# Optimization experiments

Hardware: AMD Instinct MI355X
Metric: run time of the kernel (lower is better)

The kernel has to match this reference:

```python
import jax, jax.numpy as jnp
import numpy as np

K = 50          # NEC paper uses p=50 neighbors
DELTA = 1e-3    # kernel smoothing constant


def setup_inputs() -> dict:
    key = jax.random.key(0)
    ks = jax.random.split(key, 8)
    B, D_IN, D, A, C = 512, 2, 128, 3, 200000
    s = lambda fan_in: 1.0 / np.sqrt(fan_in)
    return {
        "x": jax.random.normal(ks[0], (B, D_IN), jnp.float32),
        "W1": jax.random.normal(ks[1], (D_IN, D), jnp.float32) * s(D_IN),
        "b1": jnp.zeros((D,), jnp.float32),
        "W2": jax.random.normal(ks[2], (D, D), jnp.float32) * s(D),
        "b2": jnp.zeros((D,), jnp.float32),
        "W3": jax.random.normal(ks[3], (D, D), jnp.float32) * s(D),
        "b3": jnp.zeros((D,), jnp.float32),
        "W4": jax.random.normal(ks[4], (D, D), jnp.float32) * s(D),
        "b4": jnp.zeros((D,), jnp.float32),
        "keys": jax.random.normal(ks[5], (A, C, D), jnp.float32),
        "mem_values": jax.random.normal(ks[6], (A, C), jnp.float32),
    }


def _encode(x, W1, b1, W2, b2, W3, b3, W4, b4):
    h = jax.nn.relu(x @ W1 + b1)
    h = jax.nn.relu(h @ W2 + b2)
    h = jax.nn.relu(h @ W3 + b3)
    return h @ W4 + b4  # [B, D]


def _dnd_lookup(h, keys, mem_values):
    # h: [B, D]; keys: [A, C, D]; mem_values: [A, C]
    q2 = jnp.sum(h * h, axis=-1)                       # [B]
    k2 = jnp.sum(keys * keys, axis=-1)                 # [A, C]
    cross = jnp.einsum("bd,acd->bac", h, keys)         # [B, A, C]
    d2 = jnp.maximum(q2[:, None, None] + k2[None] - 2.0 * cross, 0.0)
    neg_d, idx = jax.lax.top_k(-d2, K)                  # [B, A, K]
    d_top = -neg_d
    w = 1.0 / (d_top + DELTA)                           # NEC kernel
    w = w / jnp.sum(w, axis=-1, keepdims=True)
    a_idx = jnp.arange(keys.shape[0])[None, :, None]    # [1, A, 1]
    v_top = mem_values[a_idx, idx]                      # gather -> [B, A, K]
    values = jnp.sum(w * v_top, axis=-1)                # [B, A]
    return values


def reference(x, W1, b1, W2, b2, W3, b3, W4, b4, keys, mem_values):
    h = _encode(x, W1, b1, W2, b2, W3, b3, W4, b4)
    values = _dnd_lookup(h, keys, mem_values)
    actions = jnp.argmax(values, axis=-1)
    return values, actions
```

## Files before the change

### kernel.cpp

```cpp
#include <hip/hip_runtime.h>
#include <hip/hip_bf16.h>
#include <math.h>

#define B_    512
#define DIM   128
#define A_    3
#define C_    200000
#define K_    50
#define DELTA 1e-3

typedef __attribute__((ext_vector_type(8))) short bf16x8;
typedef __attribute__((ext_vector_type(4))) float f32x4;

#define NBIN_A 128
#define CAP_A  1024
#define NSEG_G 128
#define TPS_G  13
#define NT_G   1563
#define HSEG   16
#define CHPS   782
#define ROWCH  12500
#define NL     16

#define AOFF_H64   0u
#define AOFF_H32   524288u
#define AOFF_HBF   786432u
#define AOFF_Q2    917504u
#define AOFF_HIST  919552u
#define AOFF_CNT   1705984u
#define AOFF_TAUB  1712128u
#define AOFF_V64   1718272u
#define AOFF_CAND  1730560u
#define AOFF_BINS  8022016u
#define NEED_A     (8022016ull + 307200000ull)

#define NBIN_B 192
#define CAP_B  768
#define BM_B   64
#define BN_B   128
#define TPC_B  16
#define CHUNK_B (TPC_B*BN_B)
#define NCH_B  ((C_ + CHUNK_B - 1)/CHUNK_B)

#define BOFF_H32   0u
#define BOFF_H64   262144u
#define BOFF_Q2    786432u
#define BOFF_K2    788480u
#define BOFF_HIST  3188480u
#define BOFF_TAU   4368128u
#define BOFF_CNT   4374272u
#define BOFF_V64   4380416u
#define BOFF_CAND  4392704u

static __device__ inline unsigned short f2bf(float x) {
    union { float f; unsigned u; } c; c.f = x;
    unsigned r = (c.u + 0x7FFFu + ((c.u >> 16) & 1u)) >> 16;
    return (unsigned short)r;
}
static __device__ inline unsigned pkbf(float a, float b) {
    __hip_bfloat162 t = __float22bfloat162_rn(make_float2(a, b));
    union { __hip_bfloat162 h; unsigned u; } cv; cv.h = t; return cv.u;
}

__global__ __launch_bounds__(128) void mlp_kernel(
    const float* __restrict__ x,
    const float* __restrict__ W1, const float* __restrict__ b1,
    const float* __restrict__ W2, const float* __restrict__ b2,
    const float* __restrict__ W3, const float* __restrict__ b3,
    const float* __restrict__ W4, const float* __restrict__ b4,
    float* __restrict__ h32, unsigned short* __restrict__ hbf,
    double* __restrict__ h64, float* __restrict__ q2)
{
    int b = blockIdx.x, t = threadIdx.x;
    __shared__ double s0[DIM], s1[DIM];
    double x0 = (double)x[b*2+0], x1 = (double)x[b*2+1];
    double h = x0*(double)W1[t] + x1*(double)W1[DIM+t] + (double)b1[t];
    s0[t] = h > 0.0 ? h : 0.0;
    __syncthreads();
    double acc = (double)b2[t];
    for (int k = 0; k < DIM; k++) acc += s0[k]*(double)W2[k*DIM+t];
    s1[t] = acc > 0.0 ? acc : 0.0;
    __syncthreads();
    acc = (double)b3[t];
    for (int k = 0; k < DIM; k++) acc += s1[k]*(double)W3[k*DIM+t];
    s0[t] = acc > 0.0 ? acc : 0.0;
    __syncthreads();
    acc = (double)b4[t];
    for (int k = 0; k < DIM; k++) acc += s0[k]*(double)W4[k*DIM+t];
    h64[b*DIM+t] = acc;
    float hf = (float)acc;
    h32[b*DIM+t] = hf;
    hbf[b*DIM+t] = f2bf(hf);
    s1[t] = acc*acc;
    __syncthreads();
    for (int s = 64; s > 0; s >>= 1) { if (t < s) s1[t] += s1[t+s]; __syncthreads(); }
    if (t == 0) q2[b] = (float)s1[0];
}

__global__ __launch_bounds__(256, 2) void gemm_bin_kernel(
    const float* __restrict__ keys, const unsigned short* __restrict__ hbf,
    const float* __restrict__ q2, unsigned char* __restrict__ bins)
{
    const int seg = blockIdx.x, my = blockIdx.y, a = blockIdx.z;
    const int b0 = my*128;
    const int tid = threadIdx.x;
    const int lane = tid & 63, w = tid >> 6;
    const int lm = lane & 15, kh = lane >> 4;
    const int wm = w & 1;
    const int wn = w >> 1;

    __shared__ short sA[128*136];
    __shared__ short sB[128*136];
    __shared__ __align__(16) float q2s[128];
    __shared__ __align__(16) float k2s[128];

    {
        int r = tid >> 1, hh = tid & 1;
        const int4* gp = (const int4*)hbf + (size_t)(b0 + r)*16 + hh*8;
        int4* dp = (int4*)&sB[r*136 + hh*64];
        #pragma unroll
        for (int q = 0; q < 8; q++) dp[q] = gp[q];
        if (tid < 128) q2s[tid] = q2[b0 + tid];
    }

    for (int t = 0; t < TPS_G; t++) {
        int nt = seg*TPS_G + t;
        if (nt >= NT_G) break;
        int n0 = nt*128;
        __syncthreads();
        {
            int r = tid >> 1, hh = tid & 1;
            int nr = n0 + r; if (nr >= C_) nr = C_-1;
            const float4* gp = (const float4*)(keys + ((size_t)a*C_ + nr)*128) + hh*16;
            float ss = 0.0f;
            int4* dp = (int4*)&sA[r*136 + hh*64];
            #pragma unroll
            for (int q = 0; q < 8; q++) {
                float4 v0 = gp[2*q], v1 = gp[2*q+1];
                ss += v0.x*v0.x + v0.y*v0.y + v0.z*v0.z + v0.w*v0.w
                    + v1.x*v1.x + v1.y*v1.y + v1.z*v1.z + v1.w*v1.w;
                int4 pk;
                pk.x = (int)pkbf(v0.x, v0.y);
                pk.y = (int)pkbf(v0.z, v0.w);
                pk.z = (int)pkbf(v1.x, v1.y);
                pk.w = (int)pkbf(v1.z, v1.w);
                dp[q] = pk;
            }
            ss += __shfl_xor(ss, 1, 64);
            if (hh == 0) k2s[r] = ss;
        }
        __syncthreads();

        f32x4 acc[4][4];
        #pragma unroll
        for (int i = 0; i < 4; i++)
            #pragma unroll
            for (int j = 0; j < 4; j++) acc[i][j] = (f32x4){0.f, 0.f, 0.f, 0.f};

        #pragma unroll
        for (int kst = 0; kst < 4; kst++) {
            bf16x8 af[4], bfv[4];
            #pragma unroll
            for (int i = 0; i < 4; i++)
                af[i] = *(const bf16x8*)&sA[(wm*64 + i*16 + lm)*136 + kst*32 + kh*8];
            #pragma unroll
            for (int j = 0; j < 4; j++)
                bfv[j] = *(const bf16x8*)&sB[(wn*64 + j*16 + lm)*136 + kst*32 + kh*8];
            #pragma unroll
            for (int i = 0; i < 4; i++)
                #pragma unroll
                for (int j = 0; j < 4; j++)
                    acc[i][j] = __builtin_amdgcn_mfma_f32_16x16x32_bf16(af[i], bfv[j], acc[i][j], 0, 0, 0);
        }

        float qv[4];
        #pragma unroll
        for (int j = 0; j < 4; j++) qv[j] = q2s[wn*64 + j*16 + lm];
        #pragma unroll
        for (int i = 0; i < 4; i++) {
            int nb = wm*64 + i*16 + kh*4;
            int n  = n0 + nb;
            float4 kb = *(const float4*)&k2s[nb];
            if (n < C_) {
                #pragma unroll
                for (int j = 0; j < 4; j++) {
                    int bl = wn*64 + j*16 + lm;
                    unsigned pk = 0;
                    #pragma unroll
                    for (int r = 0; r < 4; r++) {
                        float kr = (r==0 ? kb.x : r==1 ? kb.y : r==2 ? kb.z : kb.w);
                        float d2v = fmaf(-2.0f, acc[i][j][r], qv[j] + kr);
                        float dc  = fminf(fmaxf(d2v, 16.0f), 4095.0f);
                        unsigned u = (__float_as_uint(dc) >> 19) - 2096u;
                        pk |= u << (8*r);
                    }
                    *(unsigned*)(bins + ((size_t)(a*B_ + b0 + bl))*C_ + n) = pk;
                }
            }
        }
    }
}

__global__ __launch_bounds__(256) void histA_kernel(const unsigned char* __restrict__ bins,
                                                    unsigned* __restrict__ hist)
{
    int q = blockIdx.x;
    int seg = blockIdx.y;
    int tid = threadIdx.x;
    int a = q >> 9, b = q & 511;
    int p = b*A_ + a;
    __shared__ unsigned hs[NBIN_A*8];
    for (int i = tid; i < NBIN_A*8; i += 256) hs[i] = 0;
    __syncthreads();
    const uint4* row = (const uint4*)(bins + (size_t)q*C_);
    int ch0 = seg*CHPS, ch1 = ch0 + CHPS; if (ch1 > ROWCH) ch1 = ROWCH;
    int rep = tid & 7;
    for (int ch = ch0 + tid; ch < ch1; ch += 256) {
        uint4 v = row[ch];
        unsigned d[4] = {v.x, v.y, v.z, v.w};
        #pragma unroll
        for (int e = 0; e < 4; e++) {
            unsigned x = d[e];
            atomicAdd(&hs[((x      ) & 127u)*8 + rep], 1u);
            atomicAdd(&hs[((x >>  8) & 127u)*8 + rep], 1u);
            atomicAdd(&hs[((x >> 16) & 127u)*8 + rep], 1u);
            atomicAdd(&hs[((x >> 24) & 127u)*8 + rep], 1u);
        }
    }
    __syncthreads();
    if (tid < NBIN_A) {
        unsigned s = 0;
        #pragma unroll
        for (int r2 = 0; r2 < 8; r2++) s += hs[tid*8 + r2];
        if (s) atomicAdd(&hist[(size_t)p*NBIN_A + tid], s);
    }
}

__global__ void tauA_kernel(const unsigned* __restrict__ hist, int* __restrict__ taubin)
{
    int p = blockIdx.x*256 + threadIdx.x;
    if (p >= B_*A_) return;
    const unsigned* hp = hist + (size_t)p*NBIN_A;
    unsigned cum = 0; int jsel = NBIN_A-1;
    for (int j = 0; j < NBIN_A; j++) { cum += hp[j]; if (cum >= K_) { jsel = j; break; } }
    unsigned c1 = cum + (jsel+1 < NBIN_A ? hp[jsel+1] : 0u);
    unsigned c2 = c1  + (jsel+2 < NBIN_A ? hp[jsel+2] : 0u);
    int jt = (c2 <= 768u) ? jsel+2 : jsel+1;
    if (jt > NBIN_A-1) jt = NBIN_A-1;
    taubin[p] = jt;
}

__global__ __launch_bounds__(256) void collectA_kernel(const unsigned char* __restrict__ bins,
    const int* __restrict__ taubin, unsigned* __restrict__ cnt, int* __restrict__ cand)
{
    int q = blockIdx.x, seg = blockIdx.y, tid = threadIdx.x;
    int a = q >> 9, b = q & 511;
    int p = b*A_ + a;
    int tb = taubin[p];
    unsigned thr  = (unsigned)(tb + 1);
    unsigned addv = (128u - thr) * 0x01010101u;
    const uint4* row = (const uint4*)(bins + (size_t)q*C_);
    int ch0 = seg*CHPS, ch1 = ch0 + CHPS; if (ch1 > ROWCH) ch1 = ROWCH;
    for (int ch = ch0 + tid; ch < ch1; ch += 256) {
        uint4 v = row[ch];
        unsigned d[4] = {v.x, v.y, v.z, v.w};
        #pragma unroll
        for (int e = 0; e < 4; e++) {
            unsigned m = (d[e] + addv) & 0x80808080u;
            if (m != 0x80808080u) {
                #pragma unroll
                for (int by = 0; by < 4; by++) {
                    if (!((m >> (8*by + 7)) & 1u)) {
                        int n = ch*16 + e*4 + by;
                        unsigned pos = atomicAdd(&cnt[p], 1u);
                        if (pos < CAP_A) cand[(size_t)p*CAP_A + pos] = n;
                    }
                }
            }
        }
    }
}

__global__ __launch_bounds__(64) void select_kernel(
    const float* __restrict__ keys, const double* __restrict__ h64,
    const float* __restrict__ mem_values,
    const unsigned* __restrict__ cnt, const int* __restrict__ cand,
    float* __restrict__ out_values, double* __restrict__ val64, int cap)
{
    int p = blockIdx.x; int b = p / A_, a = p % A_;
    int lane = threadIdx.x;
    __shared__ double hd[DIM];
    __shared__ float  vsm[CAP_A];

    for (int i = lane; i < DIM; i += 64) hd[i] = h64[(size_t)b*DIM + i];
    int n = (int)cnt[p]; if (n > cap) n = cap;
    __syncthreads();

    double d2r[NL];
    #pragma unroll
    for (int s = 0; s < NL; s++) d2r[s] = 1e300;

    #pragma unroll 1
    for (int s = 0; s < NL; s++) {
        int i = s*64 + lane;
        if (i < n) {
            int c = cand[(size_t)p*cap + i];
            const float4* kr = (const float4*)(keys + ((size_t)a*C_ + c)*DIM);
            double s0 = 0.0, s1 = 0.0;
            #pragma unroll 4
            for (int kq = 0; kq < 32; kq++) {
                float4 kv = kr[kq];
                double d0 = hd[4*kq+0] - (double)kv.x;
                double d1 = hd[4*kq+1] - (double)kv.y;
                double d2 = hd[4*kq+2] - (double)kv.z;
                double d3 = hd[4*kq+3] - (double)kv.w;
                s0 += d0*d0 + d1*d1; s1 += d2*d2 + d3*d3;
            }
            double d = s0 + s1;
            unsigned long long bits = __double_as_longlong(d);
            bits = (bits & ~1023ull) | (unsigned long long)i;
            d2r[s] = __longlong_as_double(bits);
            vsm[i] = mem_values[(size_t)a*C_ + c];
        }
    }
    __syncthreads();

    double accw = 0.0, accwv = 0.0;
    for (int t = 0; t < K_; t++) {
        double best = d2r[0];
        #pragma unroll
        for (int s = 1; s < NL; s++) best = fmin(best, d2r[s]);
        #pragma unroll
        for (int off = 32; off > 0; off >>= 1) {
            double o = __shfl_xor(best, off, 64);
            best = fmin(best, o);
        }
        if (best >= 1e300) break;
        unsigned gidx = (unsigned)(__double_as_longlong(best) & 1023ull);
        int ol = gidx & 63, os = gidx >> 6;
        if (lane == ol) {
            #pragma unroll
            for (int s = 0; s < NL; s++) if (s == os) d2r[s] = 1e300;
        }
        double d = best; if (d < 0.0) d = 0.0;
        double wgt = 1.0 / (d + DELTA);
        accw += wgt; accwv += wgt * (double)vsm[gidx];
    }
    if (lane == 0) {
        double v = accwv / accw;
        out_values[p] = (float)v;
        val64[p] = v;
    }
}

__global__ void argmax_kernel(const double* __restrict__ val64, float* __restrict__ out)
{
    int b = blockIdx.x*blockDim.x + threadIdx.x;
    if (b >= B_) return;
    double v0 = val64[b*A_+0], v1 = val64[b*A_+1], v2 = val64[b*A_+2];
    int bi = 0; double bv = v0;
    if (v1 > bv) { bv = v1; bi = 1; }
    if (v2 > bv) { bv = v2; bi = 2; }
    out[B_*A_ + b] = (float)bi;
}

__global__ __launch_bounds__(256) void k2_kernel(const float* __restrict__ keys,
                                                 float* __restrict__ k2)
{
    int r = blockIdx.x*4 + (threadIdx.x >> 6);
    int lane = threadIdx.x & 63;
    float2 v = ((const float2*)keys)[(size_t)r*64 + lane];
    float s = v.x*v.x + v.y*v.y;
    #pragma unroll
    for (int off = 32; off > 0; off >>= 1) s += __shfl_down(s, off, 64);
    if (lane == 0) k2[r] = s;
}

template<int MODE>
__global__ __launch_bounds__(256) void pass_kernel(
    const float* __restrict__ keys, const float* __restrict__ h32,
    const float* __restrict__ q2,   const float* __restrict__ k2,
    unsigned* __restrict__ hist,    const float* __restrict__ tau,
    unsigned* __restrict__ cnt,     int* __restrict__ cand)
{
    const int bt = blockIdx.x;
    const int ch = blockIdx.y;
    const int a  = blockIdx.z;
    const int b0 = bt*BM_B;
    const int tid = threadIdx.x;
    const int tx = tid & 31, ty = tid >> 5;

    __shared__ float4 hs4[BM_B*33];
    __shared__ float4 ks4[BN_B*33];
    __shared__ float  q2s[BM_B];
    __shared__ float  taus[BM_B];
    __shared__ unsigned hist_s[MODE == 0 ? BM_B*NBIN_B : 1];

    #pragma unroll
    for (int q = 0; q < BM_B*32/256; q++) {
        int flat = q*256 + tid; int row = flat >> 5, kq = flat & 31;
        hs4[row*33 + kq] = ((const float4*)h32)[(size_t)(b0+row)*32 + kq];
    }
    if (tid < BM_B) {
        q2s[tid] = q2[b0+tid];
        if (MODE == 1) taus[tid] = tau[(b0+tid)*A_ + a];
    }
    if (MODE == 0) for (int i = tid; i < BM_B*NBIN_B; i += 256) hist_s[i] = 0;
    const float* __restrict__ k2g = k2 + (size_t)a*C_;

    for (int t = 0; t < TPC_B; t++) {
        int n0 = ch*CHUNK_B + t*BN_B;
        if (n0 >= C_) break;
        __syncthreads();
        #pragma unroll
        for (int q = 0; q < 16; q++) {
            int flat = q*256 + tid; int row = flat >> 5, kq = flat & 31;
            int nr = n0 + row; if (nr >= C_) nr = C_-1;
            ks4[row*33 + kq] = ((const float4*)keys)[((size_t)a*C_ + nr)*32 + kq];
        }
        __syncthreads();

        float acc[8][4];
        #pragma unroll
        for (int i = 0; i < 8; i++)
            #pragma unroll
            for (int j = 0; j < 4; j++) acc[i][j] = 0.0f;

        for (int kq = 0; kq < 32; kq++) {
            float4 hv[8], kv[4];
            #pragma unroll
            for (int i = 0; i < 8; i++) hv[i] = hs4[(ty*8+i)*33 + kq];
            #pragma unroll
            for (int j = 0; j < 4; j++) kv[j] = ks4[(j*32+tx)*33 + kq];
            #pragma unroll
            for (int i = 0; i < 8; i++)
                #pragma unroll
                for (int j = 0; j < 4; j++)
                    acc[i][j] += hv[i].x*kv[j].x + hv[i].y*kv[j].y
                               + hv[i].z*kv[j].z + hv[i].w*kv[j].w;
        }

        #pragma unroll
        for (int i = 0; i < 8; i++) {
            int bl = ty*8 + i;
            float q2b = q2s[bl];
            #pragma unroll
            for (int j = 0; j < 4; j++) {
                int n = n0 + j*32 + tx;
                if (n < C_) {
                    float d2f = fmaxf(q2b + k2g[n] - 2.0f*acc[i][j], 0.0f);
                    if (MODE == 0) {
                        int bin = (int)(__float_as_uint(d2f + 1.0f) >> 19) - 2032;
                        bin = bin < 0 ? 0 : (bin > NBIN_B-1 ? NBIN_B-1 : bin);
                        atomicAdd(&hist_s[bl*NBIN_B + bin], 1u);
                    } else {
                        if (d2f < taus[bl]) {
                            int p = (b0+bl)*A_ + a;
                            unsigned pos = atomicAdd(&cnt[p], 1u);
                            if (pos < CAP_B) cand[(size_t)p*CAP_B + pos] = n;
                        }
                    }
                }
            }
        }
    }
    if (MODE == 0) {
        __syncthreads();
        for (int i = tid; i < BM_B*NBIN_B; i += 256) {
            unsigned v = hist_s[i];
            if (v) {
                int bl = i / NBIN_B, bin = i % NBIN_B;
                atomicAdd(&hist[(size_t)((b0+bl)*A_ + a)*NBIN_B + bin], v);
            }
        }
    }
}

__global__ __launch_bounds__(256) void tauB_kernel(const unsigned* __restrict__ hist,
                                                   float* __restrict__ tau)
{
    int p = blockIdx.x*256 + threadIdx.x;
    if (p >= B_*A_) return;
    const unsigned* hp = hist + (size_t)p*NBIN_B;
    unsigned cum = 0; int jsel = NBIN_B-1;
    for (int j = 0; j < NBIN_B; j++) { cum += hp[j]; if (cum >= K_) { jsel = j; break; } }
    tau[p] = __uint_as_float((unsigned)(2034 + jsel) << 19) - 1.0f;
}

extern "C" void kernel_launch(void* const* d_in, const int* in_sizes, int n_in,
                              void* d_out, int out_size, void* d_ws, size_t ws_size,
                              hipStream_t stream)
{
    const float* x    = (const float*)d_in[0];
    const float* W1   = (const float*)d_in[1];
    const float* b1   = (const float*)d_in[2];
    const float* W2   = (const float*)d_in[3];
    const float* b2   = (const float*)d_in[4];
    const float* W3   = (const float*)d_in[5];
    const float* b3   = (const float*)d_in[6];
    const float* W4   = (const float*)d_in[7];
    const float* b4   = (const float*)d_in[8];
    const float* keys = (const float*)d_in[9];
    const float* memv = (const float*)d_in[10];

    char* ws = (char*)d_ws;

    if (ws_size >= NEED_A) {
        double*         h64  = (double*)        (ws + AOFF_H64);
        float*          h32  = (float*)         (ws + AOFF_H32);
        unsigned short* hbf  = (unsigned short*)(ws + AOFF_HBF);
        float*          q2   = (float*)         (ws + AOFF_Q2);
        unsigned*       hist = (unsigned*)      (ws + AOFF_HIST);
        unsigned*       cnt  = (unsigned*)      (ws + AOFF_CNT);
        int*            taub = (int*)           (ws + AOFF_TAUB);
        double*         v64  = (double*)        (ws + AOFF_V64);
        int*            cand = (int*)           (ws + AOFF_CAND);
        unsigned char*  bins = (unsigned char*) (ws + AOFF_BINS);

        hipMemsetAsync(ws + AOFF_HIST, 0, (AOFF_CNT + B_*A_*4) - AOFF_HIST, stream);

        mlp_kernel<<<B_, 128, 0, stream>>>(x, W1, b1, W2, b2, W3, b3, W4, b4, h32, hbf, h64, q2);
        gemm_bin_kernel<<<dim3(NSEG_G, 4, A_), 256, 0, stream>>>(keys, hbf, q2, bins);
        histA_kernel<<<dim3(B_*A_, HSEG), 256, 0, stream>>>(bins, hist);
        tauA_kernel<<<(B_*A_ + 255)/256, 256, 0, stream>>>(hist, taub);
        collectA_kernel<<<dim3(B_*A_, HSEG), 256, 0, stream>>>(bins, taub, cnt, cand);
        select_kernel<<<B_*A_, 64, 0, stream>>>(keys, h64, memv, cnt, cand, (float*)d_out, v64, CAP_A);
        argmax_kernel<<<2, 256, 0, stream>>>(v64, (float*)d_out);
    } else {
        float*          h32  = (float*)         (ws + BOFF_H32);
        double*         h64  = (double*)        (ws + BOFF_H64);
        float*          q2   = (float*)         (ws + BOFF_Q2);
        float*          k2   = (float*)         (ws + BOFF_K2);
        unsigned*       hist = (unsigned*)      (ws + BOFF_HIST);
        float*          tau  = (float*)         (ws + BOFF_TAU);
        unsigned*       cnt  = (unsigned*)      (ws + BOFF_CNT);
        double*         v64  = (double*)        (ws + BOFF_V64);
        int*            cand = (int*)           (ws + BOFF_CAND);
        unsigned short* hbf  = (unsigned short*)(ws + BOFF_CAND);

        hipMemsetAsync(ws + BOFF_HIST, 0, (BOFF_CNT + B_*A_*4) - BOFF_HIST, stream);

        mlp_kernel<<<B_, 128, 0, stream>>>(x, W1, b1, W2, b2, W3, b3, W4, b4, h32, hbf, h64, q2);
        k2_kernel<<<(A_*C_)/4, 256, 0, stream>>>(keys, k2);
        pass_kernel<0><<<dim3(B_/BM_B, NCH_B, A_), 256, 0, stream>>>(keys, h32, q2, k2, hist, nullptr, nullptr, nullptr);
        tauB_kernel<<<(B_*A_ + 255)/256, 256, 0, stream>>>(hist, tau);
        pass_kernel<1><<<dim3(B_/BM_B, NCH_B, A_), 256, 0, stream>>>(keys, h32, q2, k2, nullptr, tau, cnt, cand);
        select_kernel<<<B_*A_, 64, 0, stream>>>(keys, h64, memv, cnt, cand, (float*)d_out, v64, CAP_B);
        argmax_kernel<<<2, 256, 0, stream>>>(v64, (float*)d_out);
    }
}
```

Measured before the change: 1.098 ms.

## Pre-convert keys to bf16, async-load swizzled GEMM tiles, use per-thread byte histograms

Adds a conversion kernel that turns the fp32 keys into bf16 once and computes k2, so the GEMM kernel streams half the bytes. The GEMM loads tiles straight into LDS with global_load_lds using an XOR swizzle and no padding, and the grid is retiled. The histogram kernel replaces shared atomics with per-thread 8-bit counters that are reduced afterwards, using fewer segments per row. In exchange it adds an extra pass over the keys and a large workspace, removes the low-workspace fallback path, and each thread now covers more chunks, which risks overflowing its 8-bit counters.

```diff
diff --git a/kernel.cpp b/kernel.cpp
--- a/kernel.cpp
+++ b/kernel.cpp
@@ -14,43 +14,31 @@
 
 #define NBIN_A 128
 #define CAP_A  1024
-#define NSEG_G 128
-#define TPS_G  13
-#define NT_G   1563
 #define HSEG   16
+#define HSEGH  4
 #define CHPS   782
+#define CHPSH  3125
 #define ROWCH  12500
 #define NL     16
 
-#define AOFF_H64   0u
-#define AOFF_H32   524288u
-#define AOFF_HBF   786432u
-#define AOFF_Q2    917504u
-#define AOFF_HIST  919552u
-#define AOFF_CNT   1705984u
-#define AOFF_TAUB  1712128u
-#define AOFF_V64   1718272u
-#define AOFF_CAND  1730560u
-#define AOFF_BINS  8022016u
-#define NEED_A     (8022016ull + 307200000ull)
-
-#define NBIN_B 192
-#define CAP_B  768
-#define BM_B   64
-#define BN_B   128
-#define TPC_B  16
-#define CHUNK_B (TPC_B*BN_B)
-#define NCH_B  ((C_ + CHUNK_B - 1)/CHUNK_B)
-
-#define BOFF_H32   0u
-#define BOFF_H64   262144u
-#define BOFF_Q2    786432u
-#define BOFF_K2    788480u
-#define BOFF_HIST  3188480u
-#define BOFF_TAU   4368128u
-#define BOFF_CNT   4374272u
-#define BOFF_V64   4380416u
-#define BOFF_CAND  4392704u
+#define NSEG_G 196
+#define TPS_G  8
+#define NT_G   1563
+#define ONSEG  128
+#define OTPS   13
+
+#define OFF_H64   0u
+#define OFF_HBF   524288u
+#define OFF_Q2    655360u
+#define OFF_HIST  657408u
+#define OFF_CNT   1443840u
+#define OFF_TAUB  1449984u
+#define OFF_V64   1456128u
+#define OFF_CAND  1468416u
+#define OFF_BINS  7759872u
+#define OFF_KBF   314959872u
+#define OFF_K2    468559872u
+#define NEED_F    470959872ull
 
 static __device__ inline unsigned short f2bf(float x) {
     union { float f; unsigned u; } c; c.f = x;
@@ -60,6 +48,12 @@
 static __device__ inline unsigned pkbf(float a, float b) {
     __hip_bfloat162 t = __float22bfloat162_rn(make_float2(a, b));
     union { __hip_bfloat162 h; unsigned u; } cv; cv.h = t; return cv.u;
+}
+
+typedef __attribute__((address_space(1))) unsigned gu32_t;
+typedef __attribute__((address_space(3))) unsigned lu32_t;
+static __device__ inline void async_copy16(const void* g, void* l) {
+    __builtin_amdgcn_global_load_lds((gu32_t*)g, (lu32_t*)l, 16, 0, 0);
 }
 
 __global__ __launch_bounds__(128) void mlp_kernel(
@@ -68,8 +62,8 @@
     const float* __restrict__ W2, const float* __restrict__ b2,
     const float* __restrict__ W3, const float* __restrict__ b3,
     const float* __restrict__ W4, const float* __restrict__ b4,
-    float* __restrict__ h32, unsigned short* __restrict__ hbf,
-    double* __restrict__ h64, float* __restrict__ q2)
+    unsigned short* __restrict__ hbf, double* __restrict__ h64,
+    float* __restrict__ q2)
 {
     int b = blockIdx.x, t = threadIdx.x;
     __shared__ double s0[DIM], s1[DIM];
@@ -89,7 +83,6 @@
     for (int k = 0; k < DIM; k++) acc += s0[k]*(double)W4[k*DIM+t];
     h64[b*DIM+t] = acc;
     float hf = (float)acc;
-    h32[b*DIM+t] = hf;
     hbf[b*DIM+t] = f2bf(hf);
     s1[t] = acc*acc;
     __syncthreads();
@@ -97,9 +90,29 @@
     if (t == 0) q2[b] = (float)s1[0];
 }
 
+__global__ __launch_bounds__(256) void convert_kernel(
+    const float* __restrict__ keys, unsigned short* __restrict__ kbf,
+    float* __restrict__ k2)
+{
+    int row = blockIdx.x*16 + (threadIdx.x >> 4);
+    int t = threadIdx.x & 15;
+    const float4* src = (const float4*)(keys + (size_t)row*DIM);
+    float4 v0 = src[t*2], v1 = src[t*2+1];
+    float ss = v0.x*v0.x + v0.y*v0.y + v0.z*v0.z + v0.w*v0.w
+             + v1.x*v1.x + v1.y*v1.y + v1.z*v1.z + v1.w*v1.w;
+    int4 pk;
+    pk.x = (int)pkbf(v0.x, v0.y); pk.y = (int)pkbf(v0.z, v0.w);
+    pk.z = (int)pkbf(v1.x, v1.y); pk.w = (int)pkbf(v1.z, v1.w);
+    ((int4*)kbf)[(size_t)row*16 + t] = pk;
+    #pragma unroll
+    for (int off = 8; off > 0; off >>= 1) ss += __shfl_xor(ss, off, 16);
+    if (t == 0) k2[row] = ss;
+}
+
 __global__ __launch_bounds__(256, 2) void gemm_bin_kernel(
-    const float* __restrict__ keys, const unsigned short* __restrict__ hbf,
-    const float* __restrict__ q2, unsigned char* __restrict__ bins)
+    const unsigned short* __restrict__ kbf, const float* __restrict__ k2,
+    const unsigned short* __restrict__ hbf, const float* __restrict__ q2,
+    unsigned char* __restrict__ bins)
 {
     const int seg = blockIdx.x, my = blockIdx.y, a = blockIdx.z;
     const int b0 = my*128;
@@ -109,6 +122,114 @@
     const int wm = w & 1;
     const int wn = w >> 1;
 
+    __shared__ unsigned short sA[128*128];
+    __shared__ unsigned short sB[128*128];
+    __shared__ float q2s[128];
+
+    {
+        int r = tid >> 1, hh = tid & 1;
+        const int4* gp = (const int4*)hbf + (size_t)(b0 + r)*16;
+        #pragma unroll
+        for (int q = 0; q < 8; q++) {
+            int c = hh*8 + q;
+            int phys = c ^ (r & 15);
+            *(int4*)&sB[r*128 + phys*8] = gp[c];
+        }
+        if (tid < 128) q2s[tid] = q2[b0 + tid];
+    }
+
+    const char* gp8[8];
+    const int srow = lane >> 4;
+    const int sphys = lane & 15;
+    {
+        const char* kbase = (const char*)kbf
+            + ((size_t)a*C_ + (size_t)seg*TPS_G*128)*256;
+        #pragma unroll
+        for (int q = 0; q < 8; q++) {
+            int s = w*8 + q;
+            int row_q = s*4 + srow;
+            int lc = sphys ^ (row_q & 15);
+            gp8[q] = kbase + (size_t)row_q*256 + lc*16;
+        }
+    }
+    const int kstx = lm >> 2;
+    const int khx  = kh ^ (lm & 3);
+    const float* __restrict__ k2g = k2 + (size_t)a*C_;
+
+    for (int t = 0; t < TPS_G; t++) {
+        int nt = seg*TPS_G + t;
+        if (nt >= NT_G) break;
+        int n0 = nt*128;
+        __syncthreads();
+        #pragma unroll
+        for (int q = 0; q < 8; q++) {
+            async_copy16(gp8[q], &sA[(w*8 + q)*512]);
+            gp8[q] += 128*256;
+        }
+        __syncthreads();
+
+        f32x4 acc[4][4];
+        #pragma unroll
+        for (int i = 0; i < 4; i++)
+            #pragma unroll
+            for (int j = 0; j < 4; j++) acc[i][j] = (f32x4){0.f, 0.f, 0.f, 0.f};
+
+        #pragma unroll
+        for (int kst = 0; kst < 4; kst++) {
+            int pc8 = (4*(kst ^ kstx) + khx) * 8;
+            bf16x8 af[4], bfv[4];
+            #pragma unroll
+            for (int i = 0; i < 4; i++)
+                af[i] = *(const bf16x8*)&sA[(wm*64 + i*16 + lm)*128 + pc8];
+            #pragma unroll
+            for (int j = 0; j < 4; j++)
+                bfv[j] = *(const bf16x8*)&sB[(wn*64 + j*16 + lm)*128 + pc8];
+            #pragma unroll
+            for (int i = 0; i < 4; i++)
+                #pragma unroll
+                for (int j = 0; j < 4; j++)
+                    acc[i][j] = __builtin_amdgcn_mfma_f32_16x16x32_bf16(af[i], bfv[j], acc[i][j], 0, 0, 0);
+        }
+
+        float qv[4];
+        #pragma unroll
+        for (int j = 0; j < 4; j++) qv[j] = q2s[wn*64 + j*16 + lm];
+        #pragma unroll
+        for (int i = 0; i < 4; i++) {
+            int nb = wm*64 + i*16 + kh*4;
+            int n  = n0 + nb;
+            if (n < C_) {
+                float4 kb = *(const float4*)(k2g + n);
+                #pragma unroll
+                for (int j = 0; j < 4; j++) {
+                    int bl = wn*64 + j*16 + lm;
+                    unsigned pk = 0;
+                    #pragma unroll
+                    for (int r = 0; r < 4; r++) {
+                        float kr = (r==0 ? kb.x : r==1 ? kb.y : r==2 ? kb.z : kb.w);
+                        float d2v = fmaf(-2.0f, acc[i][j][r], qv[j] + kr);
+                        float dc  = fminf(fmaxf(d2v, 16.0f), 4095.0f);
+                        unsigned u = (__float_as_uint(dc) >> 19) - 2096u;
+                        pk |= u << (8*r);
+                    }
+                    *(unsigned*)(bins + ((size_t)(a*B_ + b0 + bl))*C_ + n) = pk;
+                }
+            }
+        }
+    }
+}
+
+__global__ __launch_bounds__(256, 2) void gemm_bin_old(
+    const float* __restrict__ keys, const unsigned short* __restrict__ hbf,
+    const float* __restrict__ q2, unsigned char* __restrict__ bins)
+{
+    const int seg = blockIdx.x, my = blockIdx.y, a = blockIdx.z;
+    const int b0 = my*128;
+    const int tid = threadIdx.x;
+    const int lane = tid & 63, w = tid >> 6;
+    const int lm = lane & 15, kh = lane >> 4;
+    const int wm = w & 1, wn = w >> 1;
+
     __shared__ short sA[128*136];
     __shared__ short sB[128*136];
     __shared__ __align__(16) float q2s[128];
@@ -123,8 +244,8 @@
         if (tid < 128) q2s[tid] = q2[b0 + tid];
     }
 
-    for (int t = 0; t < TPS_G; t++) {
-        int nt = seg*TPS_G + t;
+    for (int t = 0; t < OTPS; t++) {
+        int nt = seg*OTPS + t;
         if (nt >= NT_G) break;
         int n0 = nt*128;
         __syncthreads();
@@ -209,30 +330,54 @@
     int tid = threadIdx.x;
     int a = q >> 9, b = q & 511;
     int p = b*A_ + a;
-    __shared__ unsigned hs[NBIN_A*8];
-    for (int i = tid; i < NBIN_A*8; i += 256) hs[i] = 0;
-    __syncthreads();
+    __shared__ unsigned hs32[256*32];
+    __shared__ unsigned plo[256], phi[256];
+    unsigned char* hs8 = (unsigned char*)hs32;
+    #pragma unroll
+    for (int i = 0; i < 32; i++) hs32[tid*32 + i] = 0;
+    __syncthreads();
+
     const uint4* row = (const uint4*)(bins + (size_t)q*C_);
-    int ch0 = seg*CHPS, ch1 = ch0 + CHPS; if (ch1 > ROWCH) ch1 = ROWCH;
-    int rep = tid & 7;
+    int ch0 = seg*CHPSH, ch1 = ch0 + CHPSH; if (ch1 > ROWCH) ch1 = ROWCH;
+    unsigned swz = (unsigned)((tid & 31) << 2);
+    unsigned base = (unsigned)tid << 7;
     for (int ch = ch0 + tid; ch < ch1; ch += 256) {
         uint4 v = row[ch];
         unsigned d[4] = {v.x, v.y, v.z, v.w};
         #pragma unroll
         for (int e = 0; e < 4; e++) {
             unsigned x = d[e];
-            atomicAdd(&hs[((x      ) & 127u)*8 + rep], 1u);
-            atomicAdd(&hs[((x >>  8) & 127u)*8 + rep], 1u);
-            atomicAdd(&hs[((x >> 16) & 127u)*8 + rep], 1u);
-            atomicAdd(&hs[((x >> 24) & 127u)*8 + rep], 1u);
-        }
-    }
-    __syncthreads();
-    if (tid < NBIN_A) {
-        unsigned s = 0;
-        #pragma unroll
-        for (int r2 = 0; r2 < 8; r2++) s += hs[tid*8 + r2];
-        if (s) atomicAdd(&hist[(size_t)p*NBIN_A + tid], s);
+            hs8[base + (((x      ) & 127u) ^ swz)]++;
+            hs8[base + (((x >>  8) & 127u) ^ swz)]++;
+            hs8[base + (((x >> 16) & 127u) ^ swz)]++;
+            hs8[base + (((x >> 24) & 127u) ^ swz)]++;
+        }
+    }
+    __syncthreads();
+
+    {
+        int j = tid & 31, s = tid >> 5;
+        unsigned lo = 0, hi = 0;
+        #pragma unroll 4
+        for (int m = 0; m < 32; m++) {
+            unsigned v = hs32[(s*32 + m)*32 + (j ^ m)];
+            lo += v & 0x00FF00FFu;
+            hi += (v >> 8) & 0x00FF00FFu;
+        }
+        plo[tid] = lo; phi[tid] = hi;
+    }
+    __syncthreads();
+    if (tid < 32) {
+        int j = tid;
+        unsigned L = 0, H = 0;
+        #pragma unroll
+        for (int s = 0; s < 8; s++) { L += plo[s*32 + j]; H += phi[s*32 + j]; }
+        unsigned* hp = hist + (size_t)p*NBIN_A + 4*j;
+        unsigned c0 = L & 0xFFFFu, c1 = H & 0xFFFFu, c2 = L >> 16, c3 = H >> 16;
+        if (c0) atomicAdd(hp + 0, c0);
+        if (c1) atomicAdd(hp + 1, c1);
+        if (c2) atomicAdd(hp + 2, c2);
+        if (c3) atomicAdd(hp + 3, c3);
     }
 }
 
@@ -285,7 +430,7 @@
     const float* __restrict__ keys, const double* __restrict__ h64,
     const float* __restrict__ mem_values,
     const unsigned* __restrict__ cnt, const int* __restrict__ cand,
-    float* __restrict__ out_values, double* __restrict__ val64, int cap)
+    float* __restrict__ out_values, double* __restrict__ val64)
 {
     int p = blockIdx.x; int b = p / A_, a = p % A_;
     int lane = threadIdx.x;
@@ -293,7 +438,7 @@
     __shared__ float  vsm[CAP_A];
 
     for (int i = lane; i < DIM; i += 64) hd[i] = h64[(size_t)b*DIM + i];
-    int n = (int)cnt[p]; if (n > cap) n = cap;
+    int n = (int)cnt[p]; if (n > CAP_A) n = CAP_A;
     __syncthreads();
 
     double d2r[NL];
@@ -304,7 +449,7 @@
     for (int s = 0; s < NL; s++) {
         int i = s*64 + lane;
         if (i < n) {
-            int c = cand[(size_t)p*cap + i];
+            int c = cand[(size_t)p*CAP_A + i];
             const float4* kr = (const float4*)(keys + ((size_t)a*C_ + c)*DIM);
             double s0 = 0.0, s1 = 0.0;
             #pragma unroll 4
@@ -364,129 +509,6 @@
     out[B_*A_ + b] = (float)bi;
 }
 
-__global__ __launch_bounds__(256) void k2_kernel(const float* __restrict__ keys,
-                                                 float* __restrict__ k2)
-{
-    int r = blockIdx.x*4 + (threadIdx.x >> 6);
-    int lane = threadIdx.x & 63;
-    float2 v = ((const float2*)keys)[(size_t)r*64 + lane];
-    float s = v.x*v.x + v.y*v.y;
-    #pragma unroll
-    for (int off = 32; off > 0; off >>= 1) s += __shfl_down(s, off, 64);
-    if (lane == 0) k2[r] = s;
-}
-
-template<int MODE>
-__global__ __launch_bounds__(256) void pass_kernel(
-    const float* __restrict__ keys, const float* __restrict__ h32,
-    const float* __restrict__ q2,   const float* __restrict__ k2,
-    unsigned* __restrict__ hist,    const float* __restrict__ tau,
-    unsigned* __restrict__ cnt,     int* __restrict__ cand)
-{
-    const int bt = blockIdx.x;
-    const int ch = blockIdx.y;
-    const int a  = blockIdx.z;
-    const int b0 = bt*BM_B;
-    const int tid = threadIdx.x;
-    const int tx = tid & 31, ty = tid >> 5;
-
-    __shared__ float4 hs4[BM_B*33];
-    __shared__ float4 ks4[BN_B*33];
-    __shared__ float  q2s[BM_B];
-    __shared__ float  taus[BM_B];
-    __shared__ unsigned hist_s[MODE == 0 ? BM_B*NBIN_B : 1];
-
-    #pragma unroll
-    for (int q = 0; q < BM_B*32/256; q++) {
-        int flat = q*256 + tid; int row = flat >> 5, kq = flat & 31;
-        hs4[row*33 + kq] = ((const float4*)h32)[(size_t)(b0+row)*32 + kq];
-    }
-    if (tid < BM_B) {
-        q2s[tid] = q2[b0+tid];
-        if (MODE == 1) taus[tid] = tau[(b0+tid)*A_ + a];
-    }
-    if (MODE == 0) for (int i = tid; i < BM_B*NBIN_B; i += 256) hist_s[i] = 0;
-    const float* __restrict__ k2g = k2 + (size_t)a*C_;
-
-    for (int t = 0; t < TPC_B; t++) {
-        int n0 = ch*CHUNK_B + t*BN_B;
-        if (n0 >= C_) break;
-        __syncthreads();
-        #pragma unroll
-        for (int q = 0; q < 16; q++) {
-            int flat = q*256 + tid; int row = flat >> 5, kq = flat & 31;
-            int nr = n0 + row; if (nr >= C_) nr = C_-1;
-            ks4[row*33 + kq] = ((const float4*)keys)[((size_t)a*C_ + nr)*32 + kq];
-        }
-        __syncthreads();
-
-        float acc[8][4];
-        #pragma unroll
-        for (int i = 0; i < 8; i++)
-            #pragma unroll
-            for (int j = 0; j < 4; j++) acc[i][j] = 0.0f;
-
-        for (int kq = 0; kq < 32; kq++) {
-            float4 hv[8], kv[4];
-            #pragma unroll
-            for (int i = 0; i < 8; i++) hv[i] = hs4[(ty*8+i)*33 + kq];
-            #pragma unroll
-            for (int j = 0; j < 4; j++) kv[j] = ks4[(j*32+tx)*33 + kq];
-            #pragma unroll
-            for (int i = 0; i < 8; i++)
-                #pragma unroll
-                for (int j = 0; j < 4; j++)
-                    acc[i][j] += hv[i].x*kv[j].x + hv[i].y*kv[j].y
-                               + hv[i].z*kv[j].z + hv[i].w*kv[j].w;
-        }
-
-        #pragma unroll
-        for (int i = 0; i < 8; i++) {
-            int bl = ty*8 + i;
-            float q2b = q2s[bl];
-            #pragma unroll
-            for (int j = 0; j < 4; j++) {
-                int n = n0 + j*32 + tx;
-                if (n < C_) {
-                    float d2f = fmaxf(q2b + k2g[n] - 2.0f*acc[i][j], 0.0f);
-                    if (MODE == 0) {
-                        int bin = (int)(__float_as_uint(d2f + 1.0f) >> 19) - 2032;
-                        bin = bin < 0 ? 0 : (bin > NBIN_B-1 ? NBIN_B-1 : bin);
-                        atomicAdd(&hist_s[bl*NBIN_B + bin], 1u);
-                    } else {
-                        if (d2f < taus[bl]) {
-                            int p = (b0+bl)*A_ + a;
-                            unsigned pos = atomicAdd(&cnt[p], 1u);
-                            if (pos < CAP_B) cand[(size_t)p*CAP_B + pos] = n;
-                        }
-                    }
-                }
-            }
-        }
-    }
-    if (MODE == 0) {
-        __syncthreads();
-        for (int i = tid; i < BM_B*NBIN_B; i += 256) {
-            unsigned v = hist_s[i];
-            if (v) {
-                int bl = i / NBIN_B, bin = i % NBIN_B;
-                atomicAdd(&hist[(size_t)((b0+bl)*A_ + a)*NBIN_B + bin], v);
-            }
-        }
-    }
-}
-
-__global__ __launch_bounds__(256) void tauB_kernel(const unsigned* __restrict__ hist,
-                                                   float* __restrict__ tau)
-{
-    int p = blockIdx.x*256 + threadIdx.x;
-    if (p >= B_*A_) return;
-    const unsigned* hp = hist + (size_t)p*NBIN_B;
-    unsigned cum = 0; int jsel = NBIN_B-1;
-    for (int j = 0; j < NBIN_B; j++) { cum += hp[j]; if (cum >= K_) { jsel = j; break; } }
-    tau[p] = __uint_as_float((unsigned)(2034 + jsel) << 19) - 1.0f;
-}
-
 extern "C" void kernel_launch(void* const* d_in, const int* in_sizes, int n_in,
                               void* d_out, int out_size, void* d_ws, size_t ws_size,
                               hipStream_t stream)
@@ -504,48 +526,32 @@
     const float* memv = (const float*)d_in[10];
 
     char* ws = (char*)d_ws;
-
-    if (ws_size >= NEED_A) {
-        double*         h64  = (double*)        (ws + AOFF_H64);
-        float*          h32  = (float*)         (ws + AOFF_H32);
-        unsigned short* hbf  = (unsigned short*)(ws + AOFF_HBF);
-        float*          q2   = (float*)         (ws + AOFF_Q2);
-        unsigned*       hist = (unsigned*)      (ws + AOFF_HIST);
-        unsigned*       cnt  = (unsigned*)      (ws + AOFF_CNT);
-        int*            taub = (int*)           (ws + AOFF_TAUB);
-        double*         v64  = (double*)        (ws + AOFF_V64);
-        int*            cand = (int*)           (ws + AOFF_CAND);
-        unsigned char*  bins = (unsigned char*) (ws + AOFF_BINS);
-
-        hipMemsetAsync(ws + AOFF_HIST, 0, (AOFF_CNT + B_*A_*4) - AOFF_HIST, stream);
-
-        mlp_kernel<<<B_, 128, 0, stream>>>(x, W1, b1, W2, b2, W3, b3, W4, b4, h32, hbf, h64, q2);
-        gemm_bin_kernel<<<dim3(NSEG_G, 4, A_), 256, 0, stream>>>(keys, hbf, q2, bins);
-        histA_kernel<<<dim3(B_*A_, HSEG), 256, 0, stream>>>(bins, hist);
-        tauA_kernel<<<(B_*A_ + 255)/256, 256, 0, stream>>>(hist, taub);
-        collectA_kernel<<<dim3(B_*A_, HSEG), 256, 0, stream>>>(bins, taub, cnt, cand);
-        select_kernel<<<B_*A_, 64, 0, stream>>>(keys, h64, memv, cnt, cand, (float*)d_out, v64, CAP_A);
-        argmax_kernel<<<2, 256, 0, stream>>>(v64, (float*)d_out);
+    double*         h64  = (double*)        (ws + OFF_H64);
+    unsigned short* hbf  = (unsigned short*)(ws + OFF_HBF);
+    float*          q2   = (float*)         (ws + OFF_Q2);
+    unsigned*       hist = (unsigned*)      (ws + OFF_HIST);
+    unsigned*       cnt  = (unsigned*)      (ws + OFF_CNT);
+    int*            taub = (int*)           (ws + OFF_TAUB);
+    double*         v64  = (double*)        (ws + OFF_V64);
+    int*            cand = (int*)           (ws + OFF_CAND);
+    unsigned char*  bins = (unsigned char*) (ws + OFF_BINS);
+    unsigned short* kbf  = (unsigned short*)(ws + OFF_KBF);
+    float*          k2   = (float*)         (ws + OFF_K2);
+
+    hipMemsetAsync(ws + OFF_HIST, 0, (OFF_CNT + B_*A_*4) - OFF_HIST, stream);
+
+    mlp_kernel<<<B_, 128, 0, stream>>>(x, W1, b1, W2, b2, W3, b3, W4, b4, hbf, h64, q2);
+
+    if (ws_size >= NEED_F) {
+        convert_kernel<<<(A_*C_)/16, 256, 0, stream>>>(keys, kbf, k2);
+        gemm_bin_kernel<<<dim3(NSEG_G, 4, A_), 256, 0, stream>>>(kbf, k2, hbf, q2, bins);
     } else {
-        float*          h32  = (float*)         (ws + BOFF_H32);
-        double*         h64  = (double*)        (ws + BOFF_H64);
-        float*          q2   = (float*)         (ws + BOFF_Q2);
-        float*          k2   = (float*)         (ws + BOFF_K2);
-        unsigned*       hist = (unsigned*)      (ws + BOFF_HIST);
-        float*          tau  = (float*)         (ws + BOFF_TAU);
-        unsigned*       cnt  = (unsigned*)      (ws + BOFF_CNT);
-        double*         v64  = (double*)        (ws + BOFF_V64);
-        int*            cand = (int*)           (ws + BOFF_CAND);
-        unsigned short* hbf  = (unsigned short*)(ws + BOFF_CAND);
-
-        hipMemsetAsync(ws + BOFF_HIST, 0, (BOFF_CNT + B_*A_*4) - BOFF_HIST, stream);
-
-        mlp_kernel<<<B_, 128, 0, stream>>>(x, W1, b1, W2, b2, W3, b3, W4, b4, h32, hbf, h64, q2);
-        k2_kernel<<<(A_*C_)/4, 256, 0, stream>>>(keys, k2);
-        pass_kernel<0><<<dim3(B_/BM_B, NCH_B, A_), 256, 0, stream>>>(keys, h32, q2, k2, hist, nullptr, nullptr, nullptr);
-        tauB_kernel<<<(B_*A_ + 255)/256, 256, 0, stream>>>(hist, tau);
-        pass_kernel<1><<<dim3(B_/BM_B, NCH_B, A_), 256, 0, stream>>>(keys, h32, q2, k2, nullptr, tau, cnt, cand);
-        select_kernel<<<B_*A_, 64, 0, stream>>>(keys, h64, memv, cnt, cand, (float*)d_out, v64, CAP_B);
-        argmax_kernel<<<2, 256, 0, stream>>>(v64, (float*)d_out);
-    }
-}
+        gemm_bin_old<<<dim3(ONSEG, 4, A_), 256, 0, stream>>>(keys, hbf, q2, bins);
+    }
+
+    histA_kernel<<<dim3(B_*A_, HSEGH), 256, 0, stream>>>(bins, hist);
+    tauA_kernel<<<(B_*A_ + 255)/256, 256, 0, stream>>>(hist, taub);
+    collectA_kernel<<<dim3(B_*A_, HSEG), 256, 0, stream>>>(bins, taub, cnt, cand);
+    select_kernel<<<B_*A_, 64, 0, stream>>>(keys, h64, memv, cnt, cand, (float*)d_out, v64);
+    argmax_kernel<<<2, 256, 0, stream>>>(v64, (float*)d_out);
+}
```

Result: slower. 1.158 ms (+5.5%).
